# Kernel optimization log

Measured on AMD Instinct MI355X. Metric: run time of the kernel, lower is better.

Reference implementation:

```python
import jax, jax.numpy as jnp
import numpy as np

N, K, DIN = 2, 2048, 1024
H, DOUT = 16, 64


def setup_inputs() -> dict:
    key = jax.random.key(0)
    ks = jax.random.split(key, 12)
    c_qk = float(np.sqrt(6.0 / (DIN + DOUT)))  # per-head q/k init scale
    c_v = c_qk  # dim_q == dim_v == DOUT here
    u = lambda k, shape, c: jax.random.uniform(k, shape, jnp.float32, -c, c)
    inp = {
        "query": jax.random.normal(ks[0], (N, K, DIN), jnp.float32),
        "key": jax.random.normal(ks[1], (N, K, DIN), jnp.float32),
        "value": jax.random.normal(ks[2], (N, K, DIN), jnp.float32),
        "mask": jax.random.randint(ks[3], (N, K, K), 0, 2) > 0,  # bool (N,K,K)
        # stacked per-head projection weights: (H, DIN, DOUT), biases (H, DOUT)
        "Wq": u(ks[4], (H, DIN, DOUT), c_qk),
        "bq": u(ks[5], (H, DOUT), c_qk),
        "Wk": u(ks[6], (H, DIN, DOUT), c_qk),
        "bk": u(ks[7], (H, DOUT), c_qk),
        "Wv": u(ks[8], (H, DIN, DOUT), c_v),
        "bv": u(ks[9], (H, DOUT), c_v),
        # output projection: (H*DOUT, DIN)
        "Wp": u(ks[10], (H * DOUT, DIN), c_qk),
        "bp": u(ks[11], (DIN,), c_qk),
    }
    return inp


def reference(query, key, value, mask, Wq, bq, Wk, bk, Wv, bv, Wp, bp):
    # Per-head projections, batched over heads: (N,K,DIN) x (H,DIN,DOUT) -> (N,H,K,DOUT)
    q = jnp.einsum("nkm,hmd->nhkd", query, Wq) + bq[None, :, None, :]
    k = jnp.einsum("nkm,hmd->nhkd", key, Wk) + bk[None, :, None, :]
    v = jnp.einsum("nkm,hmd->nhkd", value, Wv) + bv[None, :, None, :]
    # scaled dot-product scores: (N,H,K,K), scaled by sqrt(per-head dim)
    scores = jnp.einsum("nhkd,nhld->nhkl", q, k) / jnp.sqrt(jnp.asarray(DOUT, q.dtype))
    scores = jnp.where(mask[:, None, :, :], jnp.asarray(-1e9, scores.dtype), scores)
    w = jax.nn.softmax(scores, axis=-1)
    y = jnp.einsum("nhkl,nhld->nhkd", w, v)  # (N,H,K,DOUT)
    # concat heads along feature dim (head order matches torch cat over head list)
    y = jnp.transpose(y, (0, 2, 1, 3)).reshape(N, K, H * DOUT)
    return y @ Wp + bp
```

## Files before the change

### kernel.cpp

```cpp
#include <hip/hip_runtime.h>
#include <hip/hip_bf16.h>
#include <stdint.h>

typedef __attribute__((ext_vector_type(8))) __bf16 bf16x8;
typedef __attribute__((ext_vector_type(4))) float floatx4;

#define NB 2
#define SEQ 2048
#define DIN 1024
#define NH 16
#define DH 64
#define DMODEL 1024
#define BQ 128
#define BK 64
#define PAD 72
#define QSCALE 0.18033688011112042f

__device__ __forceinline__ float bf2f(unsigned short u) {
    return __uint_as_float(((unsigned)u) << 16);
}
__device__ __forceinline__ unsigned short f2bf(float f) {
    unsigned u = __float_as_uint(f);
    unsigned r = (u + 0x7FFFu + ((u >> 16) & 1u)) >> 16;
    return (unsigned short)r;
}
__device__ __forceinline__ float ldin(const void* p, size_t idx, int isbf) {
    return isbf ? bf2f(((const unsigned short*)p)[idx]) : ((const float*)p)[idx];
}

__device__ __forceinline__ void gl_lds16(const void* g, void* l) {
    __builtin_amdgcn_global_load_lds(
        reinterpret_cast<__attribute__((address_space(1))) unsigned int*>(
            reinterpret_cast<uintptr_t>(g)),
        reinterpret_cast<__attribute__((address_space(3))) unsigned int*>(
            reinterpret_cast<uintptr_t>(l)),
        16, 0, 0);
}

__device__ __forceinline__ int wave_is_bf16(const void* p) {
    unsigned short u = ((const unsigned short*)p)[2 * (threadIdx.x & 63)];
    int e = (u >> 7) & 0xFF;
    int sane = (u == 0 || (e > 100 && e < 140)) ? 1 : 0;
    return __popcll(__ballot(sane)) >= 32;
}
__device__ __forceinline__ int wave_mask_is_int(const void* p) {
    int v = ((const int*)p)[threadIdx.x & 63];
    int zo = (v == 0 || v == 1) ? 1 : 0;
    return __popcll(__ballot(zo)) >= 48;
}

__global__ __launch_bounds__(256) void prep(
    const void* __restrict__ q, const void* __restrict__ k, const void* __restrict__ v,
    const void* __restrict__ mask,
    const void* __restrict__ wq, const void* __restrict__ wk,
    const void* __restrict__ wv, const void* __restrict__ wp,
    unsigned short* __restrict__ a0, unsigned short* __restrict__ a1,
    unsigned short* __restrict__ a2,
    unsigned short* __restrict__ t0, unsigned short* __restrict__ t1,
    unsigned short* __restrict__ t2, unsigned short* __restrict__ t3,
    unsigned int* __restrict__ mbits)
{
    __shared__ float xls[64][68];
    const int b = blockIdx.x;
    const int tid = threadIdx.x;
    if (b < 12288) {
        int z = b >> 12, blk = b & 4095;
        const void* src = (z == 0) ? q : (z == 1) ? k : v;
        unsigned short* dst = (z == 0) ? a0 : (z == 1) ? a1 : a2;
        int isbf = wave_is_bf16(src);
        size_t i = ((size_t)blk * 256 + tid) * 4;
        if (isbf) {
            *(ushort4*)&dst[i] = *(const ushort4*)((const unsigned short*)src + i);
        } else {
            float4 f = *(const float4*)((const float*)src + i);
            ushort4 o;
            o.x = f2bf(f.x); o.y = f2bf(f.y); o.z = f2bf(f.z); o.w = f2bf(f.w);
            *(ushort4*)&dst[i] = o;
        }
    } else if (b < 13312) {
        int blk = b - 12288;
        int w = blk * 256 + tid;
        int is_int = wave_mask_is_int(mask);
        unsigned bits = 0;
        if (is_int) {
            const int4* p = (const int4*)mask + (size_t)w * 8;
#pragma unroll
            for (int g = 0; g < 8; ++g) {
                int4 vv = p[g];
                bits |= (unsigned)(vv.x != 0) << (g * 4 + 0);
                bits |= (unsigned)(vv.y != 0) << (g * 4 + 1);
                bits |= (unsigned)(vv.z != 0) << (g * 4 + 2);
                bits |= (unsigned)(vv.w != 0) << (g * 4 + 3);
            }
        } else {
            const uint4* p = (const uint4*)mask + (size_t)w * 2;
#pragma unroll
            for (int g = 0; g < 2; ++g) {
                uint4 vv = p[g];
                unsigned ws4[4] = {vv.x, vv.y, vv.z, vv.w};
#pragma unroll
                for (int c = 0; c < 4; ++c)
#pragma unroll
                    for (int bb = 0; bb < 4; ++bb)
                        bits |= (unsigned)(((ws4[c] >> (8 * bb)) & 0xFFu) != 0)
                                << (g * 16 + c * 4 + bb);
            }
        }
        mbits[w] = bits;
    } else {
        int zb = b - 13312;
        int z = zb >> 8, t = zb & 255;
        const void* src = (z == 0) ? wq : (z == 1) ? wk : (z == 2) ? wv : wp;
        unsigned short* dst = (z == 0) ? t0 : (z == 1) ? t1 : (z == 2) ? t2 : t3;
        int isbf = wave_is_bf16(src);
        int r = tid >> 2, cs = (tid & 3) * 16;
        if (z < 3) {
            int h = t >> 4, m0 = (t & 15) * 64;
#pragma unroll
            for (int j = 0; j < 16; ++j)
                xls[r][cs + j] = ldin(src, (size_t)h * 65536 + (size_t)(m0 + r) * 64 + cs + j, isbf);
            __syncthreads();
            int d2 = tid >> 2, ms = (tid & 3) * 16;
            size_t orow = (size_t)(h * 64 + d2) * 1024 + m0 + ms;
#pragma unroll
            for (int g = 0; g < 4; ++g) {
                ushort4 o;
                o.x = f2bf(xls[ms + g * 4 + 0][d2]);
                o.y = f2bf(xls[ms + g * 4 + 1][d2]);
                o.z = f2bf(xls[ms + g * 4 + 2][d2]);
                o.w = f2bf(xls[ms + g * 4 + 3][d2]);
                *(ushort4*)&dst[orow + g * 4] = o;
            }
        } else {
            int m0 = (t >> 4) * 64, c0 = (t & 15) * 64;
#pragma unroll
            for (int j = 0; j < 16; ++j)
                xls[r][cs + j] = ldin(src, (size_t)(m0 + r) * 1024 + c0 + cs + j, isbf);
            __syncthreads();
            int d2 = tid >> 2, ms = (tid & 3) * 16;
            size_t orow = (size_t)(c0 + d2) * 1024 + m0 + ms;
#pragma unroll
            for (int g = 0; g < 4; ++g) {
                ushort4 o;
                o.x = f2bf(xls[ms + g * 4 + 0][d2]);
                o.y = f2bf(xls[ms + g * 4 + 1][d2]);
                o.z = f2bf(xls[ms + g * 4 + 2][d2]);
                o.w = f2bf(xls[ms + g * 4 + 3][d2]);
                *(ushort4*)&dst[orow + g * 4] = o;
            }
        }
    }
}

__global__ __launch_bounds__(256) void gemm_mfma(
    const unsigned short* __restrict__ A0, const unsigned short* __restrict__ A1,
    const unsigned short* __restrict__ A2,
    const unsigned short* __restrict__ B0, const unsigned short* __restrict__ B1,
    const unsigned short* __restrict__ B2,
    const void* __restrict__ bias0, const void* __restrict__ bias1,
    const void* __restrict__ bias2,
    void* __restrict__ C0, void* __restrict__ C1, void* __restrict__ C2,
    int mode0)
{
    const int z = blockIdx.z;
    const unsigned short* A  = (z == 0) ? A0 : (z == 1) ? A1 : A2;
    const unsigned short* BT = (z == 0) ? B0 : (z == 1) ? B1 : B2;
    const void* bias = (z == 0) ? bias0 : (z == 1) ? bias1 : bias2;
    void* C = (z == 0) ? C0 : (z == 1) ? C1 : C2;
    const int mode = mode0 + z;
    const int isbf = wave_is_bf16(bias);
    const float scl = (mode == 0) ? QSCALE : 1.0f;

    const int n0  = blockIdx.x * 128;
    const int m0g = blockIdx.y * 128;
    const int tid = threadIdx.x;
    const int wave = tid >> 6, lane = tid & 63;
    const int l16 = lane & 15, quad = lane >> 4;
    const int wm = wave & 1, wn = wave >> 1;

    __shared__ __align__(16) unsigned short smem[17408];
    unsigned short* As = smem;
    unsigned short* Bs = smem + 8192;

    floatx4 acc[4][4];
#pragma unroll
    for (int mt = 0; mt < 4; ++mt)
#pragma unroll
        for (int nt = 0; nt < 4; ++nt) acc[mt][nt] = floatx4{0.f, 0.f, 0.f, 0.f};

    const int lrow8 = lane >> 3;
    const int lseg  = (lane & 7) * 8;

    for (int kk = 0; kk < 1024; kk += 64) {
#pragma unroll
        for (int j = 0; j < 4; ++j) {
            int row0 = wave * 8 + j * 32;
            gl_lds16(&A[(size_t)(m0g + row0 + lrow8) * 1024 + kk + lseg], &As[row0 * 64]);
            gl_lds16(&BT[(size_t)(n0 + row0 + lrow8) * 1024 + kk + lseg], &Bs[row0 * 64]);
        }
        __syncthreads();
#pragma unroll
        for (int ks = 0; ks < 2; ++ks) {
            bf16x8 af[4], bf[4];
#pragma unroll
            for (int mt = 0; mt < 4; ++mt)
                af[mt] = *(const bf16x8*)&As[(wm * 64 + mt * 16 + l16) * 64 + ks * 32 + quad * 8];
#pragma unroll
            for (int nt = 0; nt < 4; ++nt)
                bf[nt] = *(const bf16x8*)&Bs[(wn * 64 + nt * 16 + l16) * 64 + ks * 32 + quad * 8];
#pragma unroll
            for (int mt = 0; mt < 4; ++mt)
#pragma unroll
                for (int nt = 0; nt < 4; ++nt)
                    acc[mt][nt] = __builtin_amdgcn_mfma_f32_16x16x32_bf16(af[mt], bf[nt], acc[mt][nt], 0, 0, 0);
        }
        __syncthreads();
    }

    float bv4[4];
#pragma unroll
    for (int nt = 0; nt < 4; ++nt)
        bv4[nt] = ldin(bias, n0 + wn * 64 + nt * 16 + l16, isbf);

    if (mode <= 1) {
        unsigned short* O = (unsigned short*)C;
#pragma unroll
        for (int mt = 0; mt < 4; ++mt)
#pragma unroll
            for (int reg = 0; reg < 4; ++reg) {
                int row = m0g + wm * 64 + mt * 16 + quad * 4 + reg;
                int nb = row >> 11, kq = row & (SEQ - 1);
#pragma unroll
                for (int nt = 0; nt < 4; ++nt) {
                    int c = n0 + wn * 64 + nt * 16 + l16;
                    int h = c >> 6, d = c & 63;
                    O[(((size_t)nb * NH + h) * SEQ + kq) * DH + d] =
                        f2bf((acc[mt][nt][reg] + bv4[nt]) * scl);
                }
            }
    } else if (mode == 2) {
#pragma unroll
        for (int mt = 0; mt < 4; ++mt)
#pragma unroll
            for (int nt = 0; nt < 4; ++nt)
#pragma unroll
                for (int reg = 0; reg < 4; ++reg) {
                    int m_l = wm * 64 + mt * 16 + quad * 4 + reg;
                    int c_l = wn * 64 + nt * 16 + l16;
                    smem[c_l * 136 + m_l] = f2bf(acc[mt][nt][reg] + bv4[nt]);
                }
        __syncthreads();
        unsigned short* O = (unsigned short*)C;
        int nb = m0g >> 11;
        int kq0 = m0g & (SEQ - 1);
#pragma unroll
        for (int j = 0; j < 8; ++j) {
            int i = tid + j * 256;
            int c_l = i >> 4, m8 = (i & 15) * 8;
            int cg = n0 + c_l, h = cg >> 6, d = cg & 63;
            *(bf16x8*)&O[(((size_t)nb * NH + h) * DH + d) * SEQ + kq0 + m8] =
                *(const bf16x8*)&smem[c_l * 136 + m8];
        }
    } else {
        unsigned short* Ob = (unsigned short*)C;
        float* Of = (float*)C;
#pragma unroll
        for (int mt = 0; mt < 4; ++mt)
#pragma unroll
            for (int reg = 0; reg < 4; ++reg) {
                int row = m0g + wm * 64 + mt * 16 + quad * 4 + reg;
#pragma unroll
                for (int nt = 0; nt < 4; ++nt) {
                    int c = n0 + wn * 64 + nt * 16 + l16;
                    float v = acc[mt][nt][reg] + bv4[nt];
                    if (isbf) Ob[(size_t)row * DMODEL + c] = f2bf(v);
                    else      Of[(size_t)row * DMODEL + c] = v;
                }
            }
    }
}

__global__ __launch_bounds__(512) void attn_mfma(
    const unsigned short* __restrict__ qws, const unsigned short* __restrict__ kws,
    const unsigned short* __restrict__ vtws, const unsigned int* __restrict__ mbits,
    unsigned short* __restrict__ yws)
{
    const int qt   = blockIdx.x;
    const int h    = blockIdx.y;
    const int n    = blockIdx.z;
    const int tid  = threadIdx.x;
    const int wave = tid >> 6;
    const int lane = tid & 63;
    const int l16  = lane & 15;
    const int quad = lane >> 4;

    __shared__ __align__(16) unsigned short Ks[2][BK * DH];
    __shared__ __align__(16) unsigned short VTs[2][DH * BK];
    __shared__ __align__(16) unsigned short Ps[8][16 * PAD];

    const size_t base_nh = ((size_t)n * NH + h) * SEQ * DH;
    const size_t base_vt = ((size_t)n * NH + h) * DH * SEQ;
    const int q0 = qt * BQ;
    const int qrow = wave * 16 + l16;

    const unsigned int* mrl = mbits + ((size_t)n * SEQ + q0 + qrow) * (SEQ / 32);

    const int srow8  = lane >> 3;
    const int schunk = ((lane & 7) ^ srow8) * 8;
    const int swz = l16 & 7;
    int koff[2], voff[2];
#pragma unroll
    for (int ks = 0; ks < 2; ++ks) {
        koff[ks] = l16 * DH + (((ks * 4 + quad) ^ swz) * 8);
        voff[ks] = l16 * BK + (((ks * 4 + quad) ^ swz) * 8);
    }

    bf16x8 af[2];
    {
        const unsigned short* qp = qws + base_nh + (size_t)(q0 + qrow) * DH + quad * 8;
        af[0] = *(const bf16x8*)qp;
        af[1] = *(const bf16x8*)(qp + 32);
    }

    {
        int rl = wave * 8;
        gl_lds16(&kws[base_nh + (size_t)(rl + srow8) * DH + schunk], &Ks[0][rl * DH]);
        gl_lds16(&vtws[base_vt + (size_t)(rl + srow8) * SEQ + schunk], &VTs[0][rl * BK]);
    }

    floatx4 O[4];
#pragma unroll
    for (int dt = 0; dt < 4; ++dt) O[dt] = floatx4{0.f, 0.f, 0.f, 0.f};
    float lrow = 0.f;

    __syncthreads();

    for (int it = 0; it < SEQ / BK; ++it) {
        const int cur = it & 1, nxt = cur ^ 1;
        const bool has_next = (it + 1) < (SEQ / BK);
        const int j0 = it * BK;
        const int j0n = j0 + BK;

        if (has_next) {
            int rl = wave * 8;
            gl_lds16(&kws[base_nh + (size_t)(j0n + rl + srow8) * DH + schunk], &Ks[nxt][rl * DH]);
            gl_lds16(&vtws[base_vt + (size_t)(rl + srow8) * SEQ + j0n + schunk], &VTs[nxt][rl * BK]);
        }

        uint2 mw2 = *(const uint2*)&mrl[j0 >> 5];

        bf16x8 bfK[4][2];
#pragma unroll
        for (int nt = 0; nt < 4; ++nt)
#pragma unroll
            for (int ks = 0; ks < 2; ++ks)
                bfK[nt][ks] = *(const bf16x8*)&Ks[cur][nt * 16 * DH + koff[ks]];

        float St[4][4];
#pragma unroll
        for (int nt = 0; nt < 4; ++nt) {
            floatx4 c = {0.f, 0.f, 0.f, 0.f};
            c = __builtin_amdgcn_mfma_f32_16x16x32_bf16(bfK[nt][0], af[0], c, 0, 0, 0);
            c = __builtin_amdgcn_mfma_f32_16x16x32_bf16(bfK[nt][1], af[1], c, 0, 0, 0);
            St[nt][0] = c[0]; St[nt][1] = c[1]; St[nt][2] = c[2]; St[nt][3] = c[3];
        }

        {
            unsigned wlo = mw2.x, whi = mw2.y;
#pragma unroll
            for (int nt = 0; nt < 4; ++nt) {
                unsigned w = (nt & 2) ? whi : wlo;
                int bb = (nt & 1) * 16 + quad * 4;
                float p[4];
#pragma unroll
                for (int r = 0; r < 4; ++r) {
                    int bit = (w >> (bb + r)) & 1;
                    float s = bit ? -1e9f : St[nt][r];
                    p[r] = exp2f(s);
                    lrow += p[r];
                }
                unsigned p01 = (__float_as_uint(p[0]) >> 16) | (__float_as_uint(p[1]) & 0xFFFF0000u);
                unsigned p23 = (__float_as_uint(p[2]) >> 16) | (__float_as_uint(p[3]) & 0xFFFF0000u);
                uint2 pk; pk.x = p01; pk.y = p23;
                *(uint2*)&Ps[wave][l16 * PAD + nt * 16 + quad * 4] = pk;
            }
        }

        bf16x8 pa[2], vb[4][2];
#pragma unroll
        for (int ks = 0; ks < 2; ++ks)
            pa[ks] = *(const bf16x8*)&Ps[wave][l16 * PAD + ks * 32 + quad * 8];
#pragma unroll
        for (int dt = 0; dt < 4; ++dt)
#pragma unroll
            for (int ks = 0; ks < 2; ++ks)
                vb[dt][ks] = *(const bf16x8*)&VTs[cur][dt * 16 * BK + voff[ks]];
#pragma unroll
        for (int dt = 0; dt < 4; ++dt) {
            O[dt] = __builtin_amdgcn_mfma_f32_16x16x32_bf16(pa[0], vb[dt][0], O[dt], 0, 0, 0);
            O[dt] = __builtin_amdgcn_mfma_f32_16x16x32_bf16(pa[1], vb[dt][1], O[dt], 0, 0, 0);
        }

        __syncthreads();
    }

    lrow += __shfl_xor(lrow, 16);
    lrow += __shfl_xor(lrow, 32);
#pragma unroll
    for (int r = 0; r < 4; ++r) {
        float lr = __shfl(lrow, quad * 4 + r);
        float inv = (lr > 0.f) ? 1.f / lr : 0.f;
        int row = q0 + wave * 16 + quad * 4 + r;
#pragma unroll
        for (int dt = 0; dt < 4; ++dt) {
            int col = h * DH + dt * 16 + l16;
            yws[((size_t)n * SEQ + row) * DMODEL + col] = f2bf(O[dt][r] * inv);
        }
    }
}

extern "C" void kernel_launch(void* const* d_in, const int* in_sizes, int n_in,
                              void* d_out, int out_size, void* d_ws, size_t ws_size,
                              hipStream_t stream) {
    const void* query = d_in[0];
    const void* key_  = d_in[1];
    const void* value = d_in[2];
    const void* mask  = d_in[3];
    const void* Wq = d_in[4];
    const void* bq = d_in[5];
    const void* Wk = d_in[6];
    const void* bk = d_in[7];
    const void* Wv = d_in[8];
    const void* bv = d_in[9];
    const void* Wp = d_in[10];
    const void* bp = d_in[11];

    const size_t per = (size_t)NB * NH * SEQ * DH;
    unsigned short* us = (unsigned short*)d_ws;
    unsigned short* qws  = us;
    unsigned short* kws  = us + per;
    unsigned short* vtws = us + 2 * per;
    unsigned short* abf0 = us + 3 * per;
    unsigned short* abf1 = us + 4 * per;
    unsigned short* abf2 = us + 5 * per;
    unsigned short* wt0  = us + 6 * per;
    unsigned short* wt1  = wt0 + 1048576;
    unsigned short* wt2  = wt1 + 1048576;
    unsigned short* wt3  = wt2 + 1048576;
    unsigned int* mbits  = (unsigned int*)(wt3 + 1048576);
    unsigned short* yws = abf0;

    prep<<<dim3(14336), 256, 0, stream>>>(query, key_, value, mask,
                                          Wq, Wk, Wv, Wp,
                                          abf0, abf1, abf2,
                                          wt0, wt1, wt2, wt3, mbits);
    gemm_mfma<<<dim3(8, 32, 3), 256, 0, stream>>>(abf0, abf1, abf2, wt0, wt1, wt2,
                                                  bq, bk, bv, qws, kws, vtws, 0);
    attn_mfma<<<dim3(SEQ / BQ, NH, NB), 512, 0, stream>>>(qws, kws, vtws, mbits, yws);
    gemm_mfma<<<dim3(8, 32, 1), 256, 0, stream>>>(yws, yws, yws, wt3, wt3, wt3,
                                                  bp, bp, bp, d_out, d_out, d_out, 3);
}
```

Measured before the change: 300.8 us.

## Precompute 16-bit AND masks, use hardware exp2 and MFMA row-sum in attention

Adds a kernel that expands the packed bit mask into per-element 16-bit all-ones or zero words, reusing a dead workspace buffer. The attention loop then applies the mask with a bitwise AND on bf16-converted exponentials instead of per-element bit extraction and selects. It also uses the raw hardware exp2 and computes the softmax denominator with an extra MFMA against a ones vector instead of scalar accumulation and shuffles. This cuts VALU work in the inner loop but adds an extra kernel and reads a mask 16x larger from memory on every head, which costs more bandwidth.

```diff
diff --git a/kernel.cpp b/kernel.cpp
--- a/kernel.cpp
+++ b/kernel.cpp
@@ -3,6 +3,7 @@
 #include <stdint.h>
 
 typedef __attribute__((ext_vector_type(8))) __bf16 bf16x8;
+typedef __attribute__((ext_vector_type(2))) __bf16 bf16x2;
 typedef __attribute__((ext_vector_type(4))) float floatx4;
 
 #define NB 2
@@ -152,6 +153,23 @@
     }
 }
 
+__global__ __launch_bounds__(256) void expand_mask(
+    const unsigned int* __restrict__ mbits, unsigned short* __restrict__ m16)
+{
+    int gid = blockIdx.x * 256 + threadIdx.x;
+    unsigned w = mbits[gid];
+    unsigned wrd[16];
+#pragma unroll
+    for (int i = 0; i < 16; ++i) {
+        unsigned lo = ((w >> (2 * i)) & 1u) - 1u;
+        unsigned hi = ((w >> (2 * i + 1)) & 1u) - 1u;
+        wrd[i] = (lo & 0xFFFFu) | (hi << 16);
+    }
+    uint4* dst = (uint4*)&m16[(size_t)gid * 32];
+#pragma unroll
+    for (int g = 0; g < 4; ++g) dst[g] = *(uint4*)&wrd[g * 4];
+}
+
 __global__ __launch_bounds__(256) void gemm_mfma(
     const unsigned short* __restrict__ A0, const unsigned short* __restrict__ A1,
     const unsigned short* __restrict__ A2,
@@ -282,7 +300,7 @@
 
 __global__ __launch_bounds__(512) void attn_mfma(
     const unsigned short* __restrict__ qws, const unsigned short* __restrict__ kws,
-    const unsigned short* __restrict__ vtws, const unsigned int* __restrict__ mbits,
+    const unsigned short* __restrict__ vtws, const unsigned short* __restrict__ m16,
     unsigned short* __restrict__ yws)
 {
     const int qt   = blockIdx.x;
@@ -303,7 +321,7 @@
     const int q0 = qt * BQ;
     const int qrow = wave * 16 + l16;
 
-    const unsigned int* mrl = mbits + ((size_t)n * SEQ + q0 + qrow) * (SEQ / 32);
+    const unsigned short* mrl = m16 + ((size_t)n * SEQ + q0 + qrow) * SEQ;
 
     const int srow8  = lane >> 3;
     const int schunk = ((lane & 7) ^ srow8) * 8;
@@ -314,6 +332,10 @@
         koff[ks] = l16 * DH + (((ks * 4 + quad) ^ swz) * 8);
         voff[ks] = l16 * BK + (((ks * 4 + quad) ^ swz) * 8);
     }
+
+    bf16x8 vones;
+#pragma unroll
+    for (int j = 0; j < 8; ++j) vones[j] = (__bf16)1.0f;
 
     bf16x8 af[2];
     {
@@ -331,7 +353,7 @@
     floatx4 O[4];
 #pragma unroll
     for (int dt = 0; dt < 4; ++dt) O[dt] = floatx4{0.f, 0.f, 0.f, 0.f};
-    float lrow = 0.f;
+    floatx4 Lacc = floatx4{0.f, 0.f, 0.f, 0.f};
 
     __syncthreads();
 
@@ -347,7 +369,10 @@
             gl_lds16(&vtws[base_vt + (size_t)(rl + srow8) * SEQ + j0n + schunk], &VTs[nxt][rl * BK]);
         }
 
-        uint2 mw2 = *(const uint2*)&mrl[j0 >> 5];
+        uint2 mm[4];
+#pragma unroll
+        for (int nt = 0; nt < 4; ++nt)
+            mm[nt] = *(const uint2*)&mrl[j0 + nt * 16 + quad * 4];
 
         bf16x8 bfK[4][2];
 #pragma unroll
@@ -365,25 +390,17 @@
             St[nt][0] = c[0]; St[nt][1] = c[1]; St[nt][2] = c[2]; St[nt][3] = c[3];
         }
 
-        {
-            unsigned wlo = mw2.x, whi = mw2.y;
-#pragma unroll
-            for (int nt = 0; nt < 4; ++nt) {
-                unsigned w = (nt & 2) ? whi : wlo;
-                int bb = (nt & 1) * 16 + quad * 4;
-                float p[4];
-#pragma unroll
-                for (int r = 0; r < 4; ++r) {
-                    int bit = (w >> (bb + r)) & 1;
-                    float s = bit ? -1e9f : St[nt][r];
-                    p[r] = exp2f(s);
-                    lrow += p[r];
-                }
-                unsigned p01 = (__float_as_uint(p[0]) >> 16) | (__float_as_uint(p[1]) & 0xFFFF0000u);
-                unsigned p23 = (__float_as_uint(p[2]) >> 16) | (__float_as_uint(p[3]) & 0xFFFF0000u);
-                uint2 pk; pk.x = p01; pk.y = p23;
-                *(uint2*)&Ps[wave][l16 * PAD + nt * 16 + quad * 4] = pk;
-            }
+#pragma unroll
+        for (int nt = 0; nt < 4; ++nt) {
+            bf16x2 e01, e23;
+            e01[0] = (__bf16)__builtin_amdgcn_exp2f(St[nt][0]);
+            e01[1] = (__bf16)__builtin_amdgcn_exp2f(St[nt][1]);
+            e23[0] = (__bf16)__builtin_amdgcn_exp2f(St[nt][2]);
+            e23[1] = (__bf16)__builtin_amdgcn_exp2f(St[nt][3]);
+            uint2 pk;
+            pk.x = (*(unsigned*)&e01) & mm[nt].x;
+            pk.y = (*(unsigned*)&e23) & mm[nt].y;
+            *(uint2*)&Ps[wave][l16 * PAD + nt * 16 + quad * 4] = pk;
         }
 
         bf16x8 pa[2], vb[4][2];
@@ -395,6 +412,9 @@
 #pragma unroll
             for (int ks = 0; ks < 2; ++ks)
                 vb[dt][ks] = *(const bf16x8*)&VTs[cur][dt * 16 * BK + voff[ks]];
+
+        Lacc = __builtin_amdgcn_mfma_f32_16x16x32_bf16(pa[0], vones, Lacc, 0, 0, 0);
+        Lacc = __builtin_amdgcn_mfma_f32_16x16x32_bf16(pa[1], vones, Lacc, 0, 0, 0);
 #pragma unroll
         for (int dt = 0; dt < 4; ++dt) {
             O[dt] = __builtin_amdgcn_mfma_f32_16x16x32_bf16(pa[0], vb[dt][0], O[dt], 0, 0, 0);
@@ -404,11 +424,9 @@
         __syncthreads();
     }
 
-    lrow += __shfl_xor(lrow, 16);
-    lrow += __shfl_xor(lrow, 32);
 #pragma unroll
     for (int r = 0; r < 4; ++r) {
-        float lr = __shfl(lrow, quad * 4 + r);
+        float lr = Lacc[r];
         float inv = (lr > 0.f) ? 1.f / lr : 0.f;
         int row = q0 + wave * 16 + quad * 4 + r;
 #pragma unroll
@@ -449,6 +467,7 @@
     unsigned short* wt3  = wt2 + 1048576;
     unsigned int* mbits  = (unsigned int*)(wt3 + 1048576);
     unsigned short* yws = abf0;
+    unsigned short* mask16 = abf1;
 
     prep<<<dim3(14336), 256, 0, stream>>>(query, key_, value, mask,
                                           Wq, Wk, Wv, Wp,
@@ -456,7 +475,8 @@
                                           wt0, wt1, wt2, wt3, mbits);
     gemm_mfma<<<dim3(8, 32, 3), 256, 0, stream>>>(abf0, abf1, abf2, wt0, wt1, wt2,
                                                   bq, bk, bv, qws, kws, vtws, 0);
-    attn_mfma<<<dim3(SEQ / BQ, NH, NB), 512, 0, stream>>>(qws, kws, vtws, mbits, yws);
+    expand_mask<<<dim3(1024), 256, 0, stream>>>(mbits, mask16);
+    attn_mfma<<<dim3(SEQ / BQ, NH, NB), 512, 0, stream>>>(qws, kws, vtws, mask16, yws);
     gemm_mfma<<<dim3(8, 32, 1), 256, 0, stream>>>(yws, yws, yws, wt3, wt3, wt3,
                                                   bp, bp, bp, d_out, d_out, d_out, 3);
 }
```

After: 312.7 us. 1.04x slower.

## Triple-buffer attention K/V loads with fine-grained waits and MFMA row sums

Applied to the files above, without the earlier changes.

The attention kernel goes from double to triple buffering of K/V tiles in LDS. The mask words are prefetched two iterations ahead, and __syncthreads is replaced by explicit vmcnt waits plus s_barrier so loads overlap with compute. Softmax row sums move to an MFMA against a ones vector, masked entries are zeroed directly using a hardware exp2, s_setprio is raised around the MFMA blocks, and blocks are remapped so each XCD handles contiguous heads for cache locality. The cost is more LDS per block, and the row sums are now taken from the bf16-rounded probabilities, which adds some rounding risk.

```diff
diff --git a/kernel.cpp b/kernel.cpp
--- a/kernel.cpp
+++ b/kernel.cpp
@@ -3,6 +3,7 @@
 #include <stdint.h>
 
 typedef __attribute__((ext_vector_type(8))) __bf16 bf16x8;
+typedef __attribute__((ext_vector_type(2))) __bf16 bf16x2;
 typedef __attribute__((ext_vector_type(4))) float floatx4;
 
 #define NB 2
@@ -280,22 +281,26 @@
     }
 }
 
-__global__ __launch_bounds__(512) void attn_mfma(
+__global__ __launch_bounds__(512, 4) void attn_mfma(
     const unsigned short* __restrict__ qws, const unsigned short* __restrict__ kws,
     const unsigned short* __restrict__ vtws, const unsigned int* __restrict__ mbits,
     unsigned short* __restrict__ yws)
 {
-    const int qt   = blockIdx.x;
-    const int h    = blockIdx.y;
-    const int n    = blockIdx.z;
+    const int linear = blockIdx.x + (blockIdx.y << 4) + (blockIdx.z << 8);
+    const int xcd = linear & 7, loc = linear >> 3;
+    const int hn  = (xcd << 2) + (loc >> 4);
+    const int qt  = loc & 15;
+    const int h   = hn & 15;
+    const int n   = hn >> 4;
+
     const int tid  = threadIdx.x;
     const int wave = tid >> 6;
     const int lane = tid & 63;
     const int l16  = lane & 15;
     const int quad = lane >> 4;
 
-    __shared__ __align__(16) unsigned short Ks[2][BK * DH];
-    __shared__ __align__(16) unsigned short VTs[2][DH * BK];
+    __shared__ __align__(16) unsigned short Ks[3][BK * DH];
+    __shared__ __align__(16) unsigned short VTs[3][DH * BK];
     __shared__ __align__(16) unsigned short Ps[8][16 * PAD];
 
     const size_t base_nh = ((size_t)n * NH + h) * SEQ * DH;
@@ -303,18 +308,7 @@
     const int q0 = qt * BQ;
     const int qrow = wave * 16 + l16;
 
-    const unsigned int* mrl = mbits + ((size_t)n * SEQ + q0 + qrow) * (SEQ / 32);
-
-    const int srow8  = lane >> 3;
-    const int schunk = ((lane & 7) ^ srow8) * 8;
-    const int swz = l16 & 7;
-    int koff[2], voff[2];
-#pragma unroll
-    for (int ks = 0; ks < 2; ++ks) {
-        koff[ks] = l16 * DH + (((ks * 4 + quad) ^ swz) * 8);
-        voff[ks] = l16 * BK + (((ks * 4 + quad) ^ swz) * 8);
-    }
-
+    const unsigned int* mr0 = mbits + ((size_t)n * SEQ + q0 + qrow) * (SEQ / 32);
     bf16x8 af[2];
     {
         const unsigned short* qp = qws + base_nh + (size_t)(q0 + qrow) * DH + quad * 8;
@@ -322,32 +316,47 @@
         af[1] = *(const bf16x8*)(qp + 32);
     }
 
-    {
+    const int srow8  = lane >> 3;
+    const int schunk = ((lane & 7) ^ srow8) * 8;
+    const int swz = l16 & 7;
+    int koff[2], voff[2];
+#pragma unroll
+    for (int ks = 0; ks < 2; ++ks) {
+        koff[ks] = l16 * DH + (((ks * 4 + quad) ^ swz) * 8);
+        voff[ks] = l16 * BK + (((ks * 4 + quad) ^ swz) * 8);
+    }
+
+    bf16x8 vones;
+#pragma unroll
+    for (int j = 0; j < 8; ++j) vones[j] = (__bf16)1.0f;
+
+    auto stage = [&](int b, int t) {
+        int j0t = t * BK;
         int rl = wave * 8;
-        gl_lds16(&kws[base_nh + (size_t)(rl + srow8) * DH + schunk], &Ks[0][rl * DH]);
-        gl_lds16(&vtws[base_vt + (size_t)(rl + srow8) * SEQ + schunk], &VTs[0][rl * BK]);
-    }
+        gl_lds16(&kws[base_nh + (size_t)(j0t + rl + srow8) * DH + schunk], &Ks[b][rl * DH]);
+        gl_lds16(&vtws[base_vt + (size_t)(rl + srow8) * SEQ + j0t + schunk], &VTs[b][rl * BK]);
+    };
 
     floatx4 O[4];
 #pragma unroll
     for (int dt = 0; dt < 4; ++dt) O[dt] = floatx4{0.f, 0.f, 0.f, 0.f};
-    float lrow = 0.f;
-
-    __syncthreads();
-
+    floatx4 Lacc = floatx4{0.f, 0.f, 0.f, 0.f};
+
+    stage(0, 0);
+    stage(1, 1);
+    uint2 mwC = *(const uint2*)&mr0[0];
+    uint2 mwN = *(const uint2*)&mr0[2];
+    asm volatile("s_waitcnt vmcnt(0)" ::: "memory");
+    __builtin_amdgcn_s_barrier();
+
+    int cur = 0;
     for (int it = 0; it < SEQ / BK; ++it) {
-        const int cur = it & 1, nxt = cur ^ 1;
-        const bool has_next = (it + 1) < (SEQ / BK);
-        const int j0 = it * BK;
-        const int j0n = j0 + BK;
-
-        if (has_next) {
-            int rl = wave * 8;
-            gl_lds16(&kws[base_nh + (size_t)(j0n + rl + srow8) * DH + schunk], &Ks[nxt][rl * DH]);
-            gl_lds16(&vtws[base_vt + (size_t)(rl + srow8) * SEQ + j0n + schunk], &VTs[nxt][rl * BK]);
-        }
-
-        uint2 mw2 = *(const uint2*)&mrl[j0 >> 5];
+        uint2 nA = {0, 0};
+        if (it + 2 < SEQ / BK) {
+            int b2 = cur + 2; b2 = (b2 >= 3) ? b2 - 3 : b2;
+            stage(b2, it + 2);
+            nA = *(const uint2*)&mr0[(it + 2) * 2];
+        }
 
         bf16x8 bfK[4][2];
 #pragma unroll
@@ -357,6 +366,7 @@
                 bfK[nt][ks] = *(const bf16x8*)&Ks[cur][nt * 16 * DH + koff[ks]];
 
         float St[4][4];
+        __builtin_amdgcn_s_setprio(1);
 #pragma unroll
         for (int nt = 0; nt < 4; ++nt) {
             floatx4 c = {0.f, 0.f, 0.f, 0.f};
@@ -364,26 +374,25 @@
             c = __builtin_amdgcn_mfma_f32_16x16x32_bf16(bfK[nt][1], af[1], c, 0, 0, 0);
             St[nt][0] = c[0]; St[nt][1] = c[1]; St[nt][2] = c[2]; St[nt][3] = c[3];
         }
-
-        {
-            unsigned wlo = mw2.x, whi = mw2.y;
-#pragma unroll
-            for (int nt = 0; nt < 4; ++nt) {
-                unsigned w = (nt & 2) ? whi : wlo;
-                int bb = (nt & 1) * 16 + quad * 4;
-                float p[4];
-#pragma unroll
-                for (int r = 0; r < 4; ++r) {
-                    int bit = (w >> (bb + r)) & 1;
-                    float s = bit ? -1e9f : St[nt][r];
-                    p[r] = exp2f(s);
-                    lrow += p[r];
-                }
-                unsigned p01 = (__float_as_uint(p[0]) >> 16) | (__float_as_uint(p[1]) & 0xFFFF0000u);
-                unsigned p23 = (__float_as_uint(p[2]) >> 16) | (__float_as_uint(p[3]) & 0xFFFF0000u);
-                uint2 pk; pk.x = p01; pk.y = p23;
-                *(uint2*)&Ps[wave][l16 * PAD + nt * 16 + quad * 4] = pk;
-            }
+        __builtin_amdgcn_s_setprio(0);
+
+#pragma unroll
+        for (int nt = 0; nt < 4; ++nt) {
+            unsigned w = (nt & 2) ? mwC.y : mwC.x;
+            int bb = (nt & 1) * 16 + quad * 4;
+            float p[4];
+#pragma unroll
+            for (int r = 0; r < 4; ++r) {
+                float e = __builtin_amdgcn_exp2f(St[nt][r]);
+                p[r] = ((w >> (bb + r)) & 1u) ? 0.f : e;
+            }
+            bf16x2 e01, e23;
+            e01[0] = (__bf16)p[0]; e01[1] = (__bf16)p[1];
+            e23[0] = (__bf16)p[2]; e23[1] = (__bf16)p[3];
+            uint2 pk;
+            pk.x = *(unsigned*)&e01;
+            pk.y = *(unsigned*)&e23;
+            *(uint2*)&Ps[wave][l16 * PAD + nt * 16 + quad * 4] = pk;
         }
 
         bf16x8 pa[2], vb[4][2];
@@ -395,20 +404,33 @@
 #pragma unroll
             for (int ks = 0; ks < 2; ++ks)
                 vb[dt][ks] = *(const bf16x8*)&VTs[cur][dt * 16 * BK + voff[ks]];
+
+        __builtin_amdgcn_s_setprio(1);
+        Lacc = __builtin_amdgcn_mfma_f32_16x16x32_bf16(pa[0], vones, Lacc, 0, 0, 0);
+        Lacc = __builtin_amdgcn_mfma_f32_16x16x32_bf16(pa[1], vones, Lacc, 0, 0, 0);
 #pragma unroll
         for (int dt = 0; dt < 4; ++dt) {
             O[dt] = __builtin_amdgcn_mfma_f32_16x16x32_bf16(pa[0], vb[dt][0], O[dt], 0, 0, 0);
             O[dt] = __builtin_amdgcn_mfma_f32_16x16x32_bf16(pa[1], vb[dt][1], O[dt], 0, 0, 0);
         }
-
-        __syncthreads();
-    }
-
-    lrow += __shfl_xor(lrow, 16);
-    lrow += __shfl_xor(lrow, 32);
+        __builtin_amdgcn_s_setprio(0);
+
+        if (it + 1 < SEQ / BK) {
+            if (it < SEQ / BK - 2)
+                asm volatile("s_waitcnt vmcnt(3)" ::: "memory");
+            else
+                asm volatile("s_waitcnt vmcnt(0)" ::: "memory");
+            __builtin_amdgcn_s_barrier();
+        }
+
+        cur = (cur == 2) ? 0 : cur + 1;
+        mwC = mwN;
+        mwN = nA;
+    }
+
 #pragma unroll
     for (int r = 0; r < 4; ++r) {
-        float lr = __shfl(lrow, quad * 4 + r);
+        float lr = Lacc[r];
         float inv = (lr > 0.f) ? 1.f / lr : 0.f;
         int row = q0 + wave * 16 + quad * 4 + r;
 #pragma unroll
```

Result: faster. 285.0 us (-5.2%).
